# Performance work log

Measured on AMD Instinct MI355X. Metric: run time of the kernel, lower is better.

The kernel has to match this reference:

```python
import jax, jax.numpy as jnp
import numpy as np


def _cmul(x, y):
    # complex multiply with real/imag stacked in last dim of size 2
    xr, xi = x[..., 0], x[..., 1]
    yr, yi = y[..., 0], y[..., 1]
    return jnp.stack([xr * yr - xi * yi, xr * yi + xi * yr], axis=-1)


def setup_inputs() -> dict:
    key = jax.random.key(0)
    k1, k2, k3 = jax.random.split(key, 3)
    B, N, H, W = 2, 64, 512, 512
    f_ipt = jax.random.normal(k1, (B, H, W, 2), dtype=jnp.float32)
    f_y = jax.random.normal(k2, (B, N, H, W, 2), dtype=jnp.float32)
    Hreal = jax.random.normal(k3, (N, H, W, 2), dtype=jnp.float32)
    return {"f_ipt": f_ipt, "f_y": f_y, "Hreal": Hreal, "NBFkeep": N}


def reference(f_ipt, f_y, Hreal, NBFkeep):
    # fmult: z_f = Hreal_f * ph (ab is expanded but unused in the original; f_ab is zeros)
    # broadcast: Hreal [N,H,W,2], f_ipt [B,H,W,2] -> z [B,N,H,W,2]
    z = _cmul(Hreal[None], f_ipt[:, None])
    diff = z - f_y
    # ftran('Ph'): conj(Hreal) * diff, summed over frame axis, / NBFkeep
    conjH = jnp.stack([Hreal[..., 0], -Hreal[..., 1]], axis=-1)
    g = jnp.sum(_cmul(conjH[None], diff), axis=1) / NBFkeep  # [B,H,W,2]
    return g
```

## Files before the change

### kernel.cpp

```cpp
#include <hip/hip_runtime.h>
#include <hip/hip_bf16.h>


typedef float f4 __attribute__((ext_vector_type(4)));

#define ACCUM(hv, v0, v1)                                   \
    do {                                                    \
        s0 += (hv).x * (hv).x + (hv).y * (hv).y;            \
        s1 += (hv).z * (hv).z + (hv).w * (hv).w;            \
        a00r += (hv).x * (v0).x + (hv).y * (v0).y;          \
        a00i += (hv).x * (v0).y - (hv).y * (v0).x;          \
        a01r += (hv).z * (v0).z + (hv).w * (v0).w;          \
        a01i += (hv).z * (v0).w - (hv).w * (v0).z;          \
        a10r += (hv).x * (v1).x + (hv).y * (v1).y;          \
        a10i += (hv).x * (v1).y - (hv).y * (v1).x;          \
        a11r += (hv).z * (v1).z + (hv).w * (v1).w;          \
        a11i += (hv).z * (v1).w - (hv).w * (v1).z;          \
    } while (0)

__global__ void __launch_bounds__(256) idt_fused_kernel(
    const f4* __restrict__ H4,
    const f4* __restrict__ Y4,
    const f4* __restrict__ X4,
    f4* __restrict__ O4,
    const int* __restrict__ nbf,
    int N, int P)
{
    int p = blockIdx.x * blockDim.x + threadIdx.x;
    if (p >= P) return;

    float s0 = 0.f, s1 = 0.f;
    float a00r = 0.f, a00i = 0.f, a01r = 0.f, a01i = 0.f;
    float a10r = 0.f, a10i = 0.f, a11r = 0.f, a11i = 0.f;

    const f4* hp = H4 + p;
    const f4* y0 = Y4 + p;
    const f4* y1 = Y4 + (size_t)N * P + p;

    const int G = N >> 2;

    f4 cH[4], c0[4], c1[4];
    #pragma unroll
    for (int j = 0; j < 4; ++j) {
        cH[j] = __builtin_nontemporal_load(hp + (size_t)j * P);
        c0[j] = __builtin_nontemporal_load(y0 + (size_t)j * P);
        c1[j] = __builtin_nontemporal_load(y1 + (size_t)j * P);
    }

    for (int g = 0; g < G - 1; ++g) {
        const size_t base = (size_t)(g + 1) * 4 * P;

        f4 nH[4], n0[4], n1[4];
        #pragma unroll
        for (int j = 0; j < 4; ++j) {
            nH[j] = __builtin_nontemporal_load(hp + base + (size_t)j * P);
            n0[j] = __builtin_nontemporal_load(y0 + base + (size_t)j * P);
            n1[j] = __builtin_nontemporal_load(y1 + base + (size_t)j * P);
        }

        #pragma unroll
        for (int j = 0; j < 4; ++j) ACCUM(cH[j], c0[j], c1[j]);

        #pragma unroll
        for (int j = 0; j < 4; ++j) { cH[j] = nH[j]; c0[j] = n0[j]; c1[j] = n1[j]; }
    }

    #pragma unroll
    for (int j = 0; j < 4; ++j) ACCUM(cH[j], c0[j], c1[j]);

    float inv = 1.0f / (float)nbf[0];

    f4 x0 = X4[p];
    f4 x1 = X4[(size_t)P + p];

    f4 o0, o1;
    o0.x = (x0.x * s0 - a00r) * inv;
    o0.y = (x0.y * s0 - a00i) * inv;
    o0.z = (x0.z * s1 - a01r) * inv;
    o0.w = (x0.w * s1 - a01i) * inv;

    o1.x = (x1.x * s0 - a10r) * inv;
    o1.y = (x1.y * s0 - a10i) * inv;
    o1.z = (x1.z * s1 - a11r) * inv;
    o1.w = (x1.w * s1 - a11i) * inv;

    __builtin_nontemporal_store(o0, O4 + p);
    __builtin_nontemporal_store(o1, O4 + (size_t)P + p);
}

extern "C" void kernel_launch(void* const* d_in, const int* in_sizes, int n_in,
                              void* d_out, int out_size, void* d_ws, size_t ws_size,
                              hipStream_t stream) {
    const float* f_ipt = (const float*)d_in[0];
    const float* f_y   = (const float*)d_in[1];
    const float* Hreal = (const float*)d_in[2];
    const int*   nbf   = (const int*)d_in[3];

    const int B = in_sizes[1] / in_sizes[2];
    const int N = in_sizes[1] / in_sizes[0];
    const int P = in_sizes[0] / B / 4;

    dim3 block(256);
    dim3 grid((P + block.x - 1) / block.x);
    idt_fused_kernel<<<grid, block, 0, stream>>>(
        (const f4*)Hreal, (const f4*)f_y, (const f4*)f_ipt,
        (f4*)d_out, nbf, N, P);
}
```

Measured before the change: 406.7 us.

## Split frame reduction across four waves per block with LDS combine

Each block now handles 64 pixels, and its four wavefronts each reduce a quarter of the N frames. Partial sums are combined through shared memory before a single wave writes the output. This gives four times as many blocks and more independent memory streams, to raise bandwidth utilization in a purely memory-bound kernel. It adds a shared-memory reduction and a barrier, and shortens the prefetch depth per thread.

```diff
diff --git a/kernel.cpp b/kernel.cpp
--- a/kernel.cpp
+++ b/kernel.cpp
@@ -1,5 +1,4 @@
 #include <hip/hip_runtime.h>
-#include <hip/hip_bf16.h>
 
 
 typedef float f4 __attribute__((ext_vector_type(4)));
@@ -18,7 +17,7 @@
         a11i += (hv).z * (v1).w - (hv).w * (v1).z;          \
     } while (0)
 
-__global__ void __launch_bounds__(256) idt_fused_kernel(
+__global__ void __launch_bounds__(256, 4) idt_fused_kernel(
     const f4* __restrict__ H4,
     const f4* __restrict__ Y4,
     const f4* __restrict__ X4,
@@ -26,66 +25,90 @@
     const int* __restrict__ nbf,
     int N, int P)
 {
-    int p = blockIdx.x * blockDim.x + threadIdx.x;
-    if (p >= P) return;
+    const int lane  = threadIdx.x & 63;
+    const int chunk = threadIdx.x >> 6;
+    const int p     = (blockIdx.x << 6) + lane;
+    const int pc    = p < P ? p : P - 1;
+
+    const int nPer  = N >> 2;
+    const int nBase = chunk * nPer;
 
     float s0 = 0.f, s1 = 0.f;
     float a00r = 0.f, a00i = 0.f, a01r = 0.f, a01i = 0.f;
     float a10r = 0.f, a10i = 0.f, a11r = 0.f, a11i = 0.f;
 
-    const f4* hp = H4 + p;
-    const f4* y0 = Y4 + p;
-    const f4* y1 = Y4 + (size_t)N * P + p;
+    const f4* hp = H4 + (size_t)nBase * P + pc;
+    const f4* y0 = Y4 + (size_t)nBase * P + pc;
+    const f4* y1 = Y4 + ((size_t)N + nBase) * P + pc;
 
-    const int G = N >> 2;
+    const int G = nPer >> 1;
 
-    f4 cH[4], c0[4], c1[4];
+    f4 cH[2], c0[2], c1[2];
     #pragma unroll
-    for (int j = 0; j < 4; ++j) {
+    for (int j = 0; j < 2; ++j) {
         cH[j] = __builtin_nontemporal_load(hp + (size_t)j * P);
         c0[j] = __builtin_nontemporal_load(y0 + (size_t)j * P);
         c1[j] = __builtin_nontemporal_load(y1 + (size_t)j * P);
     }
 
     for (int g = 0; g < G - 1; ++g) {
-        const size_t base = (size_t)(g + 1) * 4 * P;
+        const size_t base = (size_t)(g + 1) * 2 * P;
 
-        f4 nH[4], n0[4], n1[4];
+        f4 nH[2], n0[2], n1[2];
         #pragma unroll
-        for (int j = 0; j < 4; ++j) {
+        for (int j = 0; j < 2; ++j) {
             nH[j] = __builtin_nontemporal_load(hp + base + (size_t)j * P);
             n0[j] = __builtin_nontemporal_load(y0 + base + (size_t)j * P);
             n1[j] = __builtin_nontemporal_load(y1 + base + (size_t)j * P);
         }
 
         #pragma unroll
-        for (int j = 0; j < 4; ++j) ACCUM(cH[j], c0[j], c1[j]);
+        for (int j = 0; j < 2; ++j) ACCUM(cH[j], c0[j], c1[j]);
 
         #pragma unroll
-        for (int j = 0; j < 4; ++j) { cH[j] = nH[j]; c0[j] = n0[j]; c1[j] = n1[j]; }
+        for (int j = 0; j < 2; ++j) { cH[j] = nH[j]; c0[j] = n0[j]; c1[j] = n1[j]; }
     }
 
     #pragma unroll
-    for (int j = 0; j < 4; ++j) ACCUM(cH[j], c0[j], c1[j]);
+    for (int j = 0; j < 2; ++j) ACCUM(cH[j], c0[j], c1[j]);
 
-    float inv = 1.0f / (float)nbf[0];
+    __shared__ float red[10][4][64];
+    red[0][chunk][lane] = s0;   red[1][chunk][lane] = s1;
+    red[2][chunk][lane] = a00r; red[3][chunk][lane] = a00i;
+    red[4][chunk][lane] = a01r; red[5][chunk][lane] = a01i;
+    red[6][chunk][lane] = a10r; red[7][chunk][lane] = a10i;
+    red[8][chunk][lane] = a11r; red[9][chunk][lane] = a11i;
+    __syncthreads();
 
-    f4 x0 = X4[p];
-    f4 x1 = X4[(size_t)P + p];
+    if (chunk == 0 && p < P) {
+        #pragma unroll
+        for (int c = 1; c < 4; ++c) {
+            s0   += red[0][c][lane]; s1   += red[1][c][lane];
+            a00r += red[2][c][lane]; a00i += red[3][c][lane];
+            a01r += red[4][c][lane]; a01i += red[5][c][lane];
+            a10r += red[6][c][lane]; a10i += red[7][c][lane];
+            a11r += red[8][c][lane]; a11i += red[9][c][lane];
+        }
 
-    f4 o0, o1;
-    o0.x = (x0.x * s0 - a00r) * inv;
-    o0.y = (x0.y * s0 - a00i) * inv;
-    o0.z = (x0.z * s1 - a01r) * inv;
-    o0.w = (x0.w * s1 - a01i) * inv;
+        const float inv = 1.0f / (float)nbf[0];
 
-    o1.x = (x1.x * s0 - a10r) * inv;
-    o1.y = (x1.y * s0 - a10i) * inv;
-    o1.z = (x1.z * s1 - a11r) * inv;
-    o1.w = (x1.w * s1 - a11i) * inv;
+        f4 x0 = X4[p];
+        f4 x1 = X4[(size_t)P + p];
 
-    __builtin_nontemporal_store(o0, O4 + p);
-    __builtin_nontemporal_store(o1, O4 + (size_t)P + p);
+        f4 o0, o1;
+        o0.x = (x0.x * s0 - a00r) * inv;
+        o0.y = (x0.y * s0 - a00i) * inv;
+        o0.z = (x0.z * s1 - a01r) * inv;
+        o0.w = (x0.w * s1 - a01i) * inv;
+
+        o1.x = (x1.x * s0 - a10r) * inv;
+        o1.y = (x1.y * s0 - a10i) * inv;
+        o1.z = (x1.z * s1 - a11r) * inv;
+        o1.w = (x1.w * s1 - a11i) * inv;
+
+        __builtin_nontemporal_store(o0, O4 + p);
+        __builtin_nontemporal_store(o1, O4 + (size_t)P + p);
+    }
 }
 
 extern "C" void kernel_launch(void* const* d_in, const int* in_sizes, int n_in,
@@ -101,7 +124,7 @@
     const int P = in_sizes[0] / B / 4;
 
     dim3 block(256);
-    dim3 grid((P + block.x - 1) / block.x);
+    dim3 grid((P + 63) / 64);
     idt_fused_kernel<<<grid, block, 0, stream>>>(
         (const f4*)Hreal, (const f4*)f_y, (const f4*)f_ipt,
         (f4*)d_out, nbf, N, P);
```

Result: slower. 416.0 us (+2.3%).

## Process one complex pixel per thread with deeper 8-frame prefetch

Applied to the files above, without the earlier changes.

Each thread now handles one complex pixel (float2) instead of two (float4), which doubles the thread count. The per-batch software prefetch goes from 4 to 8 frames so more loads are in flight per thread, and launch bounds now request higher occupancy. Hreal loads switch from nontemporal to regular cached loads. The trade-off is narrower 8-byte memory accesses in place of 16-byte ones, and the code silently assumes N is divisible by 8.

```diff
diff --git a/kernel.cpp b/kernel.cpp
--- a/kernel.cpp
+++ b/kernel.cpp
@@ -1,91 +1,80 @@
 #include <hip/hip_runtime.h>
-#include <hip/hip_bf16.h>
 
 
-typedef float f4 __attribute__((ext_vector_type(4)));
+typedef float f2 __attribute__((ext_vector_type(2)));
 
-#define ACCUM(hv, v0, v1)                                   \
-    do {                                                    \
-        s0 += (hv).x * (hv).x + (hv).y * (hv).y;            \
-        s1 += (hv).z * (hv).z + (hv).w * (hv).w;            \
-        a00r += (hv).x * (v0).x + (hv).y * (v0).y;          \
-        a00i += (hv).x * (v0).y - (hv).y * (v0).x;          \
-        a01r += (hv).z * (v0).z + (hv).w * (v0).w;          \
-        a01i += (hv).z * (v0).w - (hv).w * (v0).z;          \
-        a10r += (hv).x * (v1).x + (hv).y * (v1).y;          \
-        a10i += (hv).x * (v1).y - (hv).y * (v1).x;          \
-        a11r += (hv).z * (v1).z + (hv).w * (v1).w;          \
-        a11i += (hv).z * (v1).w - (hv).w * (v1).z;          \
+#define ACCUM2(h, v0, v1)                          \
+    do {                                           \
+        s   += (h).x * (h).x + (h).y * (h).y;      \
+        a0r += (h).x * (v0).x + (h).y * (v0).y;    \
+        a0i += (h).x * (v0).y - (h).y * (v0).x;    \
+        a1r += (h).x * (v1).x + (h).y * (v1).y;    \
+        a1i += (h).x * (v1).y - (h).y * (v1).x;    \
     } while (0)
 
-__global__ void __launch_bounds__(256) idt_fused_kernel(
-    const f4* __restrict__ H4,
-    const f4* __restrict__ Y4,
-    const f4* __restrict__ X4,
-    f4* __restrict__ O4,
+__global__ void __launch_bounds__(256, 4) idt_fused_kernel(
+    const f2* __restrict__ H2,
+    const f2* __restrict__ Y2,
+    const f2* __restrict__ X2,
+    f2* __restrict__ O2,
     const int* __restrict__ nbf,
-    int N, int P)
+    int N, int Q)
 {
-    int p = blockIdx.x * blockDim.x + threadIdx.x;
-    if (p >= P) return;
+    const int q = blockIdx.x * blockDim.x + threadIdx.x;
+    if (q >= Q) return;
 
-    float s0 = 0.f, s1 = 0.f;
-    float a00r = 0.f, a00i = 0.f, a01r = 0.f, a01i = 0.f;
-    float a10r = 0.f, a10i = 0.f, a11r = 0.f, a11i = 0.f;
+    float s = 0.f;
+    float a0r = 0.f, a0i = 0.f;
+    float a1r = 0.f, a1i = 0.f;
 
-    const f4* hp = H4 + p;
-    const f4* y0 = Y4 + p;
-    const f4* y1 = Y4 + (size_t)N * P + p;
+    const f2* hp = H2 + q;
+    const f2* y0 = Y2 + q;
+    const f2* y1 = Y2 + (size_t)N * Q + q;
 
-    const int G = N >> 2;
+    const int G = N >> 3;
 
-    f4 cH[4], c0[4], c1[4];
+    f2 cH[8], c0[8], c1[8];
     #pragma unroll
-    for (int j = 0; j < 4; ++j) {
-        cH[j] = __builtin_nontemporal_load(hp + (size_t)j * P);
-        c0[j] = __builtin_nontemporal_load(y0 + (size_t)j * P);
-        c1[j] = __builtin_nontemporal_load(y1 + (size_t)j * P);
+    for (int j = 0; j < 8; ++j) {
+        cH[j] = hp[(size_t)j * Q];
+        c0[j] = __builtin_nontemporal_load(y0 + (size_t)j * Q);
+        c1[j] = __builtin_nontemporal_load(y1 + (size_t)j * Q);
     }
 
     for (int g = 0; g < G - 1; ++g) {
-        const size_t base = (size_t)(g + 1) * 4 * P;
+        const size_t base = (size_t)(g + 1) * 8 * Q;
 
-        f4 nH[4], n0[4], n1[4];
+        f2 nH[8], n0[8], n1[8];
         #pragma unroll
-        for (int j = 0; j < 4; ++j) {
-            nH[j] = __builtin_nontemporal_load(hp + base + (size_t)j * P);
-            n0[j] = __builtin_nontemporal_load(y0 + base + (size_t)j * P);
-            n1[j] = __builtin_nontemporal_load(y1 + base + (size_t)j * P);
+        for (int j = 0; j < 8; ++j) {
+            nH[j] = hp[base + (size_t)j * Q];
+            n0[j] = __builtin_nontemporal_load(y0 + base + (size_t)j * Q);
+            n1[j] = __builtin_nontemporal_load(y1 + base + (size_t)j * Q);
         }
 
         #pragma unroll
-        for (int j = 0; j < 4; ++j) ACCUM(cH[j], c0[j], c1[j]);
+        for (int j = 0; j < 8; ++j) ACCUM2(cH[j], c0[j], c1[j]);
 
         #pragma unroll
-        for (int j = 0; j < 4; ++j) { cH[j] = nH[j]; c0[j] = n0[j]; c1[j] = n1[j]; }
+        for (int j = 0; j < 8; ++j) { cH[j] = nH[j]; c0[j] = n0[j]; c1[j] = n1[j]; }
     }
 
     #pragma unroll
-    for (int j = 0; j < 4; ++j) ACCUM(cH[j], c0[j], c1[j]);
+    for (int j = 0; j < 8; ++j) ACCUM2(cH[j], c0[j], c1[j]);
 
-    float inv = 1.0f / (float)nbf[0];
+    const float inv = 1.0f / (float)nbf[0];
 
-    f4 x0 = X4[p];
-    f4 x1 = X4[(size_t)P + p];
+    f2 x0 = X2[q];
+    f2 x1 = X2[(size_t)Q + q];
 
-    f4 o0, o1;
-    o0.x = (x0.x * s0 - a00r) * inv;
-    o0.y = (x0.y * s0 - a00i) * inv;
-    o0.z = (x0.z * s1 - a01r) * inv;
-    o0.w = (x0.w * s1 - a01i) * inv;
+    f2 o0, o1;
+    o0.x = (x0.x * s - a0r) * inv;
+    o0.y = (x0.y * s - a0i) * inv;
+    o1.x = (x1.x * s - a1r) * inv;
+    o1.y = (x1.y * s - a1i) * inv;
 
-    o1.x = (x1.x * s0 - a10r) * inv;
-    o1.y = (x1.y * s0 - a10i) * inv;
-    o1.z = (x1.z * s1 - a11r) * inv;
-    o1.w = (x1.w * s1 - a11i) * inv;
-
-    __builtin_nontemporal_store(o0, O4 + p);
-    __builtin_nontemporal_store(o1, O4 + (size_t)P + p);
+    __builtin_nontemporal_store(o0, O2 + q);
+    __builtin_nontemporal_store(o1, O2 + (size_t)Q + q);
 }
 
 extern "C" void kernel_launch(void* const* d_in, const int* in_sizes, int n_in,
@@ -98,11 +87,11 @@
 
     const int B = in_sizes[1] / in_sizes[2];
     const int N = in_sizes[1] / in_sizes[0];
-    const int P = in_sizes[0] / B / 4;
+    const int Q = in_sizes[0] / B / 2;
 
     dim3 block(256);
-    dim3 grid((P + block.x - 1) / block.x);
+    dim3 grid((Q + block.x - 1) / block.x);
     idt_fused_kernel<<<grid, block, 0, stream>>>(
-        (const f4*)Hreal, (const f4*)f_y, (const f4*)f_ipt,
-        (f4*)d_out, nbf, N, P);
+        (const f2*)Hreal, (const f2*)f_y, (const f2*)f_ipt,
+        (f2*)d_out, nbf, N, Q);
 }
```

Result: slower. 418.8 us (+3.0%).
